# Kernel optimization log

Measured on AMD Instinct MI355X. Metric: run time of the kernel, lower is better.

The kernel has to match this reference:

```python
import jax, jax.numpy as jnp
import numpy as np

C1 = 0.01 ** 2
C2 = 0.03 ** 2
EPS = 1e-8


def _box3(t):
    # 3x3 mean filter, zero padding (SAME), NCHW, 1 channel.
    k = jnp.full((1, 1, 3, 3), 1.0 / 9.0, dtype=t.dtype)
    return jax.lax.conv_general_dilated(
        t, k, window_strides=(1, 1), padding=((1, 1), (1, 1)),
        dimension_numbers=("NCHW", "OIHW", "NCHW"))


def setup_inputs() -> dict:
    key = jax.random.key(0)
    k1, k2 = jax.random.split(key)
    shape = (32, 1, 1024, 1024)
    x = jax.random.uniform(k1, shape, dtype=jnp.float32)
    y = jax.random.uniform(k2, shape, dtype=jnp.float32)
    return {"x": x, "y": y}


def reference(x, y):
    mu_x = _box3(x)
    mu_y = _box3(y)
    sigma_x = _box3(x * x) - mu_x * mu_x
    sigma_y = _box3(y * y) - mu_y * mu_y
    sigma_xy = _box3(x * y) - mu_x * mu_y
    ssim_map = ((2.0 * mu_x * mu_y + C1) * (2.0 * sigma_xy + C2)
                / ((mu_x ** 2 + mu_y ** 2 + C1) * (sigma_x + sigma_y + C2) + EPS))
    return 1.0 - jnp.mean(ssim_map)
```

## Files before the change

### kernel.cpp

```cpp
#include <hip/hip_runtime.h>

#define IMG_H 1024
#define IMG_W 1024
#define RPB   8
#define TPB   256

struct HS { float x[4], y[4], xx[4], yy[4], xy[4]; };

__device__ __forceinline__ void zero_hs(HS& h)
{
#pragma unroll
    for (int j = 0; j < 4; ++j) { h.x[j]=0.f; h.y[j]=0.f; h.xx[j]=0.f; h.yy[j]=0.f; h.xy[j]=0.f; }
}

__device__ __forceinline__ void hsum6(float xl, float4 xv, float xr6,
                                      float yl, float4 yv, float yr6, HS& h)
{
    float xs[6] = { xl, xv.x, xv.y, xv.z, xv.w, xr6 };
    float ys[6] = { yl, yv.x, yv.y, yv.z, yv.w, yr6 };

    float pxx[6], pyy[6], pxy[6];
#pragma unroll
    for (int k = 0; k < 6; ++k) {
        pxx[k] = xs[k] * xs[k];
        pyy[k] = ys[k] * ys[k];
        pxy[k] = xs[k] * ys[k];
    }
#pragma unroll
    for (int j = 0; j < 4; ++j) {
        h.x[j]  = xs[j]  + xs[j + 1]  + xs[j + 2];
        h.y[j]  = ys[j]  + ys[j + 1]  + ys[j + 2];
        h.xx[j] = pxx[j] + pxx[j + 1] + pxx[j + 2];
        h.yy[j] = pyy[j] + pyy[j + 1] + pyy[j + 2];
        h.xy[j] = pxy[j] + pxy[j + 1] + pxy[j + 2];
    }
}

__device__ __forceinline__ void accum(const HS& A, const HS& B, const HS& C, float& acc)
{
    const float c1s  = 81.0f * 1e-4f;
    const float c2s  = 81.0f * 9e-4f;
    const float epss = 6561.0f * 1e-8f;
#pragma unroll
    for (int j = 0; j < 4; ++j) {
        const float sx  = A.x[j]  + B.x[j]  + C.x[j];
        const float sy  = A.y[j]  + B.y[j]  + C.y[j];
        const float sxx = A.xx[j] + B.xx[j] + C.xx[j];
        const float syy = A.yy[j] + B.yy[j] + C.yy[j];
        const float sxy = A.xy[j] + B.xy[j] + C.xy[j];

        const float t1 = sx * sy;
        const float t2 = fmaf(sx, sx, sy * sy);
        const float s2 = sxx + syy;
        const float An = fmaf(2.0f, t1, c1s);
        const float Bn = fmaf(-2.0f, t1, fmaf(18.0f, sxy, c2s));
        const float Xd = t2 + c1s;
        const float Yd = fmaf(9.0f, s2, c2s - t2);
        const float den = fmaf(Xd, Yd, epss);
        const float num = An * Bn;
        acc = fmaf(num, __builtin_amdgcn_rcpf(den), acc);
    }
}

__global__ __launch_bounds__(TPB, 4)
void ssim_map_sum_kernel(const float* __restrict__ x,
                         const float* __restrict__ y,
                         float* __restrict__ part)
{
    const int rb = blockIdx.x;
    const int n  = blockIdx.y;
    const int r0 = rb * RPB;
    const int c  = (int)threadIdx.x * 4;

    const int   cl = (c > 0) ? c - 1 : 0;
    const int   cr = (c + 4 < IMG_W) ? c + 4 : IMG_W - 1;
    const float lm = (c > 0) ? 1.0f : 0.0f;
    const float rm = (c + 4 < IMG_W) ? 1.0f : 0.0f;

    const float* xi = x + (size_t)n * IMG_H * IMG_W;
    const float* yi = y + (size_t)n * IMG_H * IMG_W;

    HS hA, hB, hC;

    if (r0 > 0) {
        const float* xr = xi + (size_t)(r0 - 1) * IMG_W;
        const float* yr = yi + (size_t)(r0 - 1) * IMG_W;
        hsum6(xr[cl] * lm, *reinterpret_cast<const float4*>(xr + c), xr[cr] * rm,
              yr[cl] * lm, *reinterpret_cast<const float4*>(yr + c), yr[cr] * rm, hA);
    } else {
        zero_hs(hA);
    }
    {
        const float* xr = xi + (size_t)r0 * IMG_W;
        const float* yr = yi + (size_t)r0 * IMG_W;
        hsum6(xr[cl] * lm, *reinterpret_cast<const float4*>(xr + c), xr[cr] * rm,
              yr[cl] * lm, *reinterpret_cast<const float4*>(yr + c), yr[cr] * rm, hB);
    }

    float4 pxA, pyA, pxB, pyB, pxC, pyC;
    float  xlA, xrA, ylA, yrA, xlB, xrB, ylB, yrB, xlC, xrC, ylC, yrC;

#define LOADBUF(row, S)                                                        \
    {                                                                          \
        const float* xr_ = xi + (size_t)(row) * IMG_W;                         \
        const float* yr_ = yi + (size_t)(row) * IMG_W;                         \
        px##S = *reinterpret_cast<const float4*>(xr_ + c);                     \
        py##S = *reinterpret_cast<const float4*>(yr_ + c);                     \
        xl##S = xr_[cl]; xr##S = xr_[cr];                                      \
        yl##S = yr_[cl]; yr##S = yr_[cr];                                      \
    }

    LOADBUF(r0 + 1, A)
    LOADBUF(r0 + 2, B)

    float acc = 0.0f;

#define CONSUME(S, H)                                                          \
    hsum6(xl##S * lm, px##S, xr##S * rm, yl##S * lm, py##S, yr##S * rm, H);

     LOADBUF(r0 + 3, C) CONSUME(A, hC) accum(hA, hB, hC, acc);
     LOADBUF(r0 + 4, A) CONSUME(B, hA) accum(hB, hC, hA, acc);
     LOADBUF(r0 + 5, B) CONSUME(C, hB) accum(hC, hA, hB, acc);
     LOADBUF(r0 + 6, C) CONSUME(A, hC) accum(hA, hB, hC, acc);
     LOADBUF(r0 + 7, A) CONSUME(B, hA) accum(hB, hC, hA, acc);
     {
        const int rr = (r0 + 8 < IMG_H) ? r0 + 8 : IMG_H - 1;
        LOADBUF(rr, B)
        CONSUME(C, hB) accum(hC, hA, hB, acc);
    }
     CONSUME(A, hC) accum(hA, hB, hC, acc);
    {
        const float rwm = (r0 + 8 < IMG_H) ? 1.0f : 0.0f;
        float4 xv = pxB, yv = pyB;
        xv.x *= rwm; xv.y *= rwm; xv.z *= rwm; xv.w *= rwm;
        yv.x *= rwm; yv.y *= rwm; yv.z *= rwm; yv.w *= rwm;
        hsum6(xlB * (lm * rwm), xv, xrB * (rm * rwm),
              ylB * (lm * rwm), yv, yrB * (rm * rwm), hA);
        accum(hB, hC, hA, acc);
    }
#undef CONSUME
#undef LOADBUF

#pragma unroll
    for (int off = 32; off > 0; off >>= 1)
        acc += __shfl_down(acc, off);

    __shared__ float red[TPB / 64];
    const int lane = (int)threadIdx.x & 63;
    const int wave = (int)threadIdx.x >> 6;
    if (lane == 0) red[wave] = acc;
    __syncthreads();
    if (threadIdx.x == 0) {
        float s = 0.0f;
#pragma unroll
        for (int w = 0; w < TPB / 64; ++w) s += red[w];
        part[blockIdx.y * gridDim.x + blockIdx.x] = s;
    }
}

__global__ __launch_bounds__(256)
void ssim_finalize_kernel(const float* __restrict__ part, int nparts,
                          float* __restrict__ out, float inv_count)
{
    float s = 0.0f;
    for (int i = (int)threadIdx.x; i < nparts; i += 256)
        s += part[i];
#pragma unroll
    for (int off = 32; off > 0; off >>= 1)
        s += __shfl_down(s, off);

    __shared__ float red[4];
    const int lane = (int)threadIdx.x & 63;
    const int wave = (int)threadIdx.x >> 6;
    if (lane == 0) red[wave] = s;
    __syncthreads();
    if (threadIdx.x == 0) {
        float t = red[0] + red[1] + red[2] + red[3];
        out[0] = 1.0f - t * inv_count;
    }
}

extern "C" void kernel_launch(void* const* d_in, const int* in_sizes, int n_in,
                              void* d_out, int out_size, void* d_ws, size_t ws_size,
                              hipStream_t stream)
{
    const float* x = (const float*)d_in[0];
    const float* y = (const float*)d_in[1];
    float* out  = (float*)d_out;
    float* part = (float*)d_ws;

    const long long total = (long long)in_sizes[0];
    const int N = (int)(total / ((long long)IMG_H * IMG_W));
    const int nparts = (IMG_H / RPB) * N;

    dim3 grid(IMG_H / RPB, N);
    ssim_map_sum_kernel<<<grid, TPB, 0, stream>>>(x, y, part);

    ssim_finalize_kernel<<<1, 256, 0, stream>>>(part, nparts, out, 1.0f / (float)total);
}
```

Measured before the change: 283.9 us.

## Stream rows into an LDS ring buffer via async global-to-LDS loads

Each 8-row block now copies its input rows into a 4-slot shared-memory ring buffer with global_load_lds, issuing loads two rows ahead and waiting with vmcnt plus a barrier before each row is consumed. Left and right halo values come from neighbouring threads' float4 entries in LDS instead of extra scalar global loads per row. The aim is to overlap memory latency with compute and cut redundant global requests. In exchange it adds a block-wide barrier per row and uses 32 KB of LDS per block, which may limit occupancy.

```diff
diff --git a/kernel.cpp b/kernel.cpp
--- a/kernel.cpp
+++ b/kernel.cpp
@@ -67,95 +67,91 @@
                          const float* __restrict__ y,
                          float* __restrict__ part)
 {
+    __shared__ float sbuf[4][2][IMG_W];
+
     const int rb = blockIdx.x;
     const int n  = blockIdx.y;
     const int r0 = rb * RPB;
-    const int c  = (int)threadIdx.x * 4;
+    const int t  = (int)threadIdx.x;
+    const int wv = t >> 6;
+    const int ln = t & 63;
+    const int c  = t * 4;
 
-    const int   cl = (c > 0) ? c - 1 : 0;
-    const int   cr = (c + 4 < IMG_W) ? c + 4 : IMG_W - 1;
     const float lm = (c > 0) ? 1.0f : 0.0f;
     const float rm = (c + 4 < IMG_W) ? 1.0f : 0.0f;
+    const int   tl = (t > 0) ? t - 1 : 0;
+    const int   tr = (t < TPB - 1) ? t + 1 : TPB - 1;
 
     const float* xi = x + (size_t)n * IMG_H * IMG_W;
     const float* yi = y + (size_t)n * IMG_H * IMG_W;
 
-    HS hA, hB, hC;
-
-    if (r0 > 0) {
-        const float* xr = xi + (size_t)(r0 - 1) * IMG_W;
-        const float* yr = yi + (size_t)(r0 - 1) * IMG_W;
-        hsum6(xr[cl] * lm, *reinterpret_cast<const float4*>(xr + c), xr[cr] * rm,
-              yr[cl] * lm, *reinterpret_cast<const float4*>(yr + c), yr[cr] * rm, hA);
-    } else {
-        zero_hs(hA);
-    }
-    {
-        const float* xr = xi + (size_t)r0 * IMG_W;
-        const float* yr = yi + (size_t)r0 * IMG_W;
-        hsum6(xr[cl] * lm, *reinterpret_cast<const float4*>(xr + c), xr[cr] * rm,
-              yr[cl] * lm, *reinterpret_cast<const float4*>(yr + c), yr[cr] * rm, hB);
+#define STAGE(j)                                                                  \
+    {                                                                             \
+        const int rr_ = (r0 - 1 + (j) < 0) ? 0                                    \
+                      : ((r0 - 1 + (j) > IMG_H - 1) ? IMG_H - 1 : r0 - 1 + (j));  \
+        const size_t go_ = (size_t)rr_ * IMG_W + (size_t)(wv * 256 + ln * 4);     \
+        __builtin_amdgcn_global_load_lds(                                         \
+            (const __attribute__((address_space(1))) void*)(xi + go_),            \
+            (__attribute__((address_space(3))) void*)&sbuf[(j) & 3][0][wv * 256], \
+            16, 0, 0);                                                            \
+        __builtin_amdgcn_global_load_lds(                                         \
+            (const __attribute__((address_space(1))) void*)(yi + go_),            \
+            (__attribute__((address_space(3))) void*)&sbuf[(j) & 3][1][wv * 256], \
+            16, 0, 0);                                                            \
     }
 
-    float4 pxA, pyA, pxB, pyB, pxC, pyC;
-    float  xlA, xrA, ylA, yrA, xlB, xrB, ylB, yrB, xlC, xrC, ylC, yrC;
-
-#define LOADBUF(row, S)                                                        \
-    {                                                                          \
-        const float* xr_ = xi + (size_t)(row) * IMG_W;                         \
-        const float* yr_ = yi + (size_t)(row) * IMG_W;                         \
-        px##S = *reinterpret_cast<const float4*>(xr_ + c);                     \
-        py##S = *reinterpret_cast<const float4*>(yr_ + c);                     \
-        xl##S = xr_[cl]; xr##S = xr_[cr];                                      \
-        yl##S = yr_[cl]; yr##S = yr_[cr];                                      \
+#define CONSUME(j, H, S)                                                          \
+    {                                                                             \
+        const float4* bx_ = reinterpret_cast<const float4*>(&sbuf[(j) & 3][0][0]);\
+        const float4* by_ = reinterpret_cast<const float4*>(&sbuf[(j) & 3][1][0]);\
+        float4 xo_ = bx_[t], yo_ = by_[t];                                        \
+        float4 xn_ = bx_[tl], yn_ = by_[tl];                                      \
+        float4 xp_ = bx_[tr], yp_ = by_[tr];                                      \
+        const float s_ = (S);                                                     \
+        xo_.x *= s_; xo_.y *= s_; xo_.z *= s_; xo_.w *= s_;                       \
+        yo_.x *= s_; yo_.y *= s_; yo_.z *= s_; yo_.w *= s_;                       \
+        hsum6(xn_.w * (lm * s_), xo_, xp_.x * (rm * s_),                          \
+              yn_.w * (lm * s_), yo_, yp_.x * (rm * s_), H);                      \
     }
 
-    LOADBUF(r0 + 1, A)
-    LOADBUF(r0 + 2, B)
+#define WAITV(N) asm volatile("s_waitcnt vmcnt(" #N ")" ::: "memory")
+#define BAR()    __builtin_amdgcn_s_barrier()
 
+    STAGE(0)
+    STAGE(1)
+
+    HS hA, hB, hC;
     float acc = 0.0f;
 
-#define CONSUME(S, H)                                                          \
-    hsum6(xl##S * lm, px##S, xr##S * rm, yl##S * lm, py##S, yr##S * rm, H);
-
-     LOADBUF(r0 + 3, C) CONSUME(A, hC) accum(hA, hB, hC, acc);
-     LOADBUF(r0 + 4, A) CONSUME(B, hA) accum(hB, hC, hA, acc);
-     LOADBUF(r0 + 5, B) CONSUME(C, hB) accum(hC, hA, hB, acc);
-     LOADBUF(r0 + 6, C) CONSUME(A, hC) accum(hA, hB, hC, acc);
-     LOADBUF(r0 + 7, A) CONSUME(B, hA) accum(hB, hC, hA, acc);
+     STAGE(2) WAITV(4); BAR(); CONSUME(0, hA, 1.0f)
+              if (r0 == 0) zero_hs(hA);
+     STAGE(3) WAITV(4); BAR(); CONSUME(1, hB, 1.0f)
+     STAGE(4) WAITV(4); BAR(); CONSUME(2, hC, 1.0f) accum(hA, hB, hC, acc);
+     STAGE(5) WAITV(4); BAR(); CONSUME(3, hA, 1.0f) accum(hB, hC, hA, acc);
+     STAGE(6) WAITV(4); BAR(); CONSUME(4, hB, 1.0f) accum(hC, hA, hB, acc);
+     STAGE(7) WAITV(4); BAR(); CONSUME(5, hC, 1.0f) accum(hA, hB, hC, acc);
+     STAGE(8) WAITV(4); BAR(); CONSUME(6, hA, 1.0f) accum(hB, hC, hA, acc);
+     STAGE(9) WAITV(4); BAR(); CONSUME(7, hB, 1.0f) accum(hC, hA, hB, acc);
+              WAITV(2); BAR(); CONSUME(8, hC, 1.0f) accum(hA, hB, hC, acc);
      {
-        const int rr = (r0 + 8 < IMG_H) ? r0 + 8 : IMG_H - 1;
-        LOADBUF(rr, B)
-        CONSUME(C, hB) accum(hC, hA, hB, acc);
+        const float rwm = (r0 + 8 < IMG_H) ? 1.0f : 0.0f;
+                   WAITV(0); BAR(); CONSUME(9, hA, rwm)     accum(hB, hC, hA, acc);
     }
-     CONSUME(A, hC) accum(hA, hB, hC, acc);
-    {
-        const float rwm = (r0 + 8 < IMG_H) ? 1.0f : 0.0f;
-        float4 xv = pxB, yv = pyB;
-        xv.x *= rwm; xv.y *= rwm; xv.z *= rwm; xv.w *= rwm;
-        yv.x *= rwm; yv.y *= rwm; yv.z *= rwm; yv.w *= rwm;
-        hsum6(xlB * (lm * rwm), xv, xrB * (rm * rwm),
-              ylB * (lm * rwm), yv, yrB * (rm * rwm), hA);
-        accum(hB, hC, hA, acc);
-    }
+#undef STAGE
 #undef CONSUME
-#undef LOADBUF
+#undef WAITV
+#undef BAR
 
 #pragma unroll
     for (int off = 32; off > 0; off >>= 1)
         acc += __shfl_down(acc, off);
 
-    __shared__ float red[TPB / 64];
-    const int lane = (int)threadIdx.x & 63;
-    const int wave = (int)threadIdx.x >> 6;
-    if (lane == 0) red[wave] = acc;
     __syncthreads();
-    if (threadIdx.x == 0) {
-        float s = 0.0f;
-#pragma unroll
-        for (int w = 0; w < TPB / 64; ++w) s += red[w];
-        part[blockIdx.y * gridDim.x + blockIdx.x] = s;
-    }
+    float* red = &sbuf[0][0][0];
+    if (ln == 0) red[wv] = acc;
+    __syncthreads();
+    if (t == 0)
+        part[blockIdx.y * gridDim.x + blockIdx.x] = red[0] + red[1] + red[2] + red[3];
 }
 
 __global__ __launch_bounds__(256)
```

Result: no change. 283.4 us (-0.2%).
